# Kernel optimization log

Hardware: AMD Instinct MI355X
Metric: run time of the kernel (lower is better)

## Reference

```python
import jax, jax.numpy as jnp
import numpy as np

N_NODES = 100000
N_EDGES = 20000
N_PAIRS = 640000
IN_CH = 128
HEADS = 4
OUT_CH = 32


def setup_inputs() -> dict:
    key = jax.random.key(0)
    k1, k2, k3, k4, k5 = jax.random.split(key, 5)
    X = jax.random.normal(k1, (N_NODES, IN_CH), dtype=jnp.float32)
    # nn.Linear(in, H*C, bias=False); stored as [in, H*C] so X0 = X @ W
    W = jax.random.normal(k2, (IN_CH, HEADS * OUT_CH), dtype=jnp.float32) * (1.0 / np.sqrt(IN_CH))
    stdv = (6.0 / (HEADS + OUT_CH)) ** 0.5
    att_e = jax.random.uniform(k3, (1, HEADS, OUT_CH), dtype=jnp.float32, minval=-stdv, maxval=stdv)
    vertex = jax.random.randint(k4, (N_PAIRS,), 0, N_NODES, dtype=jnp.int64)
    edges = jax.random.randint(k5, (N_PAIRS,), 0, N_EDGES, dtype=jnp.int64)
    return {"X": X, "W": W, "att_e": att_e, "vertex": vertex, "edges": edges}


def reference(X, W, att_e, vertex, edges):
    N = X.shape[0]
    H, C = HEADS, OUT_CH
    X0 = X @ W                                  # [N, H*C]
    Xv_hc = X0.reshape(N, H, C)
    Xve = Xv_hc[vertex]                          # [M, H, C] gather
    # scatter-mean over hyperedges
    esum = jax.ops.segment_sum(Xve, edges, num_segments=N_EDGES)
    ecnt = jax.ops.segment_sum(jnp.ones((Xve.shape[0],), X.dtype), edges, num_segments=N_EDGES)
    Xe = esum / jnp.maximum(ecnt, 1.0)[:, None, None]   # [E, H, C]
    alpha_e = (Xe * att_e).sum(-1)               # [E, H]
    a_ev = alpha_e[edges]                        # [M, H]
    alpha = jax.nn.leaky_relu(a_ev, 0.01)
    # per-vertex softmax over incident hyperedges
    amax = jax.ops.segment_max(alpha, vertex, num_segments=N)
    alpha = jnp.exp(alpha - amax[vertex])
    asum = jax.ops.segment_sum(alpha, vertex, num_segments=N)
    alpha = alpha / (asum[vertex] + 1e-8)
    Xev = Xe[edges] * alpha[:, :, None]          # [M, H, C]
    Xv = jax.ops.segment_sum(Xev, vertex, num_segments=N)
    return Xv.reshape(N, H * C) + X0
```

## Files before the change

kernel.cpp:

```cpp
#include <hip/hip_runtime.h>
#include <hip/hip_bf16.h>

#define N_NODES 100000
#define N_EDGES 20000
#define N_PAIRS 640000
#define CH 128
#define HEADS 4
#define MAXDV 32

#define NG_GEMM 1563
#define NCHUNK 125
#define ECHUNK 5120
#define EW 5120
#define VWR 5000
#define NRANGE 5
#define VBIN_R 20000

#define OFF_X0H   0UL
#define OFF_XEH   25600000UL
#define OFF_LRE   30720000UL
#define OFF_LRV5  31360000UL
#define OFF_BLKE  34560000UL
#define OFF_BLKV  37120000UL
#define OFF_GSE   49620000UL
#define OFF_GSV   49722400UL
#define OFF_WT    50222400UL
#define OFF_ALPHA 50255168UL
#define OFF_OFFE  50575168UL
#define OFF_ENDE  50657088UL
#define OFF_OFFV  50739008UL
#define OFF_ENDV  51139008UL
#define OFF_PIDXE 51539008UL
#define OFF_PIDXV 54099008UL
#define OFF_TOT   56659008UL
#define ZERO_BYTES 8UL

typedef __attribute__((ext_vector_type(8))) short bf16x8;
typedef __attribute__((ext_vector_type(4))) float f32x4;

__device__ inline short f2bf(float f) {
    __hip_bfloat16 h = __float2bfloat16(f);
    return reinterpret_cast<short&>(h);
}
__device__ inline float bflo(unsigned w) { return __uint_as_float(w << 16); }
__device__ inline float bfhi(unsigned w) { return __uint_as_float(w & 0xffff0000u); }

__global__ __launch_bounds__(256) void k_wprep(const float* __restrict__ W,
                                               short* __restrict__ Wt) {
    const int idx = blockIdx.x * 256 + threadIdx.x;
    const int n = idx >> 7, k = idx & 127;
    Wt[n * CH + k] = f2bf(W[k * CH + n]);
}

__device__ inline void gemm_body(int gb, const float* __restrict__ X,
                                 const short* __restrict__ Wt,
                                 short* __restrict__ X0h) {
    const int t = threadIdx.x;
    const int wave = t >> 6, lane = t & 63;
    const int r0 = gb * 64 + (wave >> 1) * 32;
    const int c0 = (wave & 1) * 64;
    const int lrow = lane & 15, lk8 = (lane >> 4) * 8;
    const int row0 = min(r0 + lrow, N_NODES - 1);
    const int row1 = min(r0 + 16 + lrow, N_NODES - 1);
    const float* px0 = &X[(size_t)row0 * CH + lk8];
    const float* px1 = &X[(size_t)row1 * CH + lk8];
    const short* pw0 = &Wt[(size_t)(c0 + lrow) * CH + lk8];

    f32x4 acc[2][4] = {};

    float4 xa[2][2]; bf16x8 bb[4];
    xa[0][0] = *(const float4*)(px0); xa[0][1] = *(const float4*)(px0 + 4);
    xa[1][0] = *(const float4*)(px1); xa[1][1] = *(const float4*)(px1 + 4);
#pragma unroll
    for (int n = 0; n < 4; ++n) bb[n] = *(const bf16x8*)(pw0 + n * 16 * CH);

#pragma unroll
    for (int kk = 0; kk < 4; ++kk) {
        float4 xn[2][2]; bf16x8 bn[4];
        if (kk < 3) {
            const int ks = (kk + 1) * 32;
            xn[0][0] = *(const float4*)(px0 + ks); xn[0][1] = *(const float4*)(px0 + ks + 4);
            xn[1][0] = *(const float4*)(px1 + ks); xn[1][1] = *(const float4*)(px1 + ks + 4);
#pragma unroll
            for (int n = 0; n < 4; ++n) bn[n] = *(const bf16x8*)(pw0 + n * 16 * CH + ks);
        }
        bf16x8 a[2];
#pragma unroll
        for (int m = 0; m < 2; ++m) {
            a[m][0] = f2bf(xa[m][0].x); a[m][1] = f2bf(xa[m][0].y);
            a[m][2] = f2bf(xa[m][0].z); a[m][3] = f2bf(xa[m][0].w);
            a[m][4] = f2bf(xa[m][1].x); a[m][5] = f2bf(xa[m][1].y);
            a[m][6] = f2bf(xa[m][1].z); a[m][7] = f2bf(xa[m][1].w);
        }
#pragma unroll
        for (int m = 0; m < 2; ++m)
#pragma unroll
            for (int n = 0; n < 4; ++n)
                acc[m][n] = __builtin_amdgcn_mfma_f32_16x16x32_bf16(a[m], bb[n], acc[m][n], 0, 0, 0);
        if (kk < 3) {
#pragma unroll
            for (int m = 0; m < 2; ++m) { xa[m][0] = xn[m][0]; xa[m][1] = xn[m][1]; }
#pragma unroll
            for (int n = 0; n < 4; ++n) bb[n] = bn[n];
        }
    }

#pragma unroll
    for (int m = 0; m < 2; ++m) {
#pragma unroll
        for (int reg = 0; reg < 4; ++reg) {
            const int row = r0 + m * 16 + (lane >> 4) * 4 + reg;
            if (row < N_NODES) {
#pragma unroll
                for (int n = 0; n < 4; ++n)
                    X0h[(size_t)row * CH + c0 + n * 16 + (lane & 15)] = f2bf(acc[m][n][reg]);
            }
        }
    }
}

__global__ __launch_bounds__(256) void k_phase1(const float* __restrict__ X,
                                                const short* __restrict__ Wt,
                                                short* __restrict__ X0h,
                                                const int* __restrict__ vertex,
                                                const int* __restrict__ edges,
                                                unsigned char* __restrict__ lrank_e,
                                                unsigned char* __restrict__ lrank_v5,
                                                unsigned int* __restrict__ blkcnt_e,
                                                unsigned int* __restrict__ blkcnt_v) {
    __shared__ unsigned int hist[EW];
    const int bid = blockIdx.x;
    const int t = threadIdx.x;

    if (bid < NRANGE * NCHUNK) {
        const int r = bid % NRANGE, c = bid / NRANGE;
        for (int i = t; i < VWR; i += 256) hist[i] = 0;
        __syncthreads();
        const int base = c * ECHUNK;
        const int vmin = r * VBIN_R;
        unsigned char* __restrict__ lr = lrank_v5 + (size_t)r * N_PAIRS;
#pragma unroll
        for (int it = 0; it < 20; ++it) {
            const int m = base + it * 256 + t;
            const int loc = vertex[m] - vmin;
            if ((unsigned)loc < (unsigned)VBIN_R) {
                const unsigned sh = (unsigned)(loc & 3) * 8u;
                unsigned old = atomicAdd(&hist[loc >> 2], 1u << sh);
                lr[m] = (unsigned char)((old >> sh) & 0xffu);
            }
        }
        __syncthreads();
        unsigned int* dst = &blkcnt_v[(size_t)(r * NCHUNK + c) * VWR];
        for (int w = t; w < VWR; w += 256) dst[w] = hist[w];
        return;
    }
    if (bid < NRANGE * NCHUNK + NCHUNK) {
        const int c = bid - NRANGE * NCHUNK;
        for (int i = t; i < EW; i += 256) hist[i] = 0;
        __syncthreads();
        const int base = c * ECHUNK;
#pragma unroll
        for (int it = 0; it < 20; ++it) {
            const int m = base + it * 256 + t;
            const int e = edges[m];
            const unsigned sh = (unsigned)(e & 3) * 8u;
            unsigned old = atomicAdd(&hist[e >> 2], 1u << sh);
            lrank_e[m] = (unsigned char)((old >> sh) & 0xffu);
        }
        __syncthreads();
        unsigned int* dst = &blkcnt_e[(size_t)c * EW];
        for (int w = t; w < EW; w += 256) dst[w] = hist[w];
        return;
    }
    gemm_body(bid - (NRANGE * NCHUNK + NCHUNK), X, Wt, X0h);
}

__global__ __launch_bounds__(256) void k_scan_p1(const unsigned int* __restrict__ blkcnt_e,
                                                 const unsigned int* __restrict__ blkcnt_v,
                                                 unsigned int* __restrict__ gse,
                                                 unsigned int* __restrict__ gsv) {
    const int bid = blockIdx.x;
    if (bid < 25) {
        const int gid = bid * 256 + threadIdx.x;
        const int g = gid / 1280, w4 = gid % 1280;
        uint4 s = {0, 0, 0, 0};
#pragma unroll 5
        for (int i = 0; i < 25; ++i) {
            uint4 c = *(const uint4*)&blkcnt_e[(size_t)(g * 25 + i) * EW + w4 * 4];
            s.x += c.x; s.y += c.y; s.z += c.z; s.w += c.w;
        }
        *(uint4*)&gse[g * EW + w4 * 4] = s;
        return;
    }
    const int vid = (bid - 25) * 256 + threadIdx.x;
    if (vid >= 25 * (VWR / 4)) return;
    const int g = vid / (VWR / 4), w4 = vid % (VWR / 4);
    const int r = g / 5, cg = g % 5;
    uint4 s = {0, 0, 0, 0};
#pragma unroll 5
    for (int i = 0; i < 25; ++i) {
        uint4 c = *(const uint4*)&blkcnt_v[(size_t)(r * NCHUNK + cg * 25 + i) * VWR + w4 * 4];
        s.x += c.x; s.y += c.y; s.z += c.z; s.w += c.w;
    }
    *(uint4*)&gsv[g * VWR + w4 * 4] = s;
}

__global__ __launch_bounds__(256) void k_p2o(unsigned int* __restrict__ gse,
                                             unsigned int* __restrict__ gsv,
                                             int* __restrict__ off_e,
                                             int* __restrict__ end_e,
                                             int* __restrict__ off_v,
                                             int* __restrict__ end_v,
                                             int* __restrict__ totals) {
    __shared__ int s[256];
    __shared__ int base;
    const int bid = blockIdx.x, t = threadIdx.x;

    unsigned run = 0;
    int t0 = 0, t1 = 0, t2 = 0, t3 = 0;
    int binbase = -1;
    int* off; int* end; int* total;

    if (bid < 20) {
        const int w = bid * 256 + t;
#pragma unroll
        for (int g = 0; g < 5; ++g) {
            unsigned c = gse[g * EW + w];
            gse[g * EW + w] = run;
            run += c;
        }
        t0 = run & 255; t1 = (run >> 8) & 255; t2 = (run >> 16) & 255; t3 = run >> 24;
        binbase = 4 * w;
        off = off_e; end = end_e; total = &totals[0];
    } else {
        const int id = (bid - 20) * 256 + t;
        if (id < NRANGE * VWR) {
            const int r = id / VWR, w = id % VWR;
#pragma unroll
            for (int g = r * 5; g < r * 5 + 5; ++g) {
                unsigned c = gsv[g * VWR + w];
                gsv[g * VWR + w] = run;
                run += c;
            }
            t0 = run & 255; t1 = (run >> 8) & 255; t2 = (run >> 16) & 255; t3 = run >> 24;
            binbase = r * VBIN_R + 4 * w;
        }
        off = off_v; end = end_v; total = &totals[1];
    }

    const int mysum = t0 + t1 + t2 + t3;
    s[t] = mysum;
    __syncthreads();
    for (int d = 1; d < 256; d <<= 1) {
        int x = (t >= d) ? s[t - d] : 0;
        __syncthreads();
        s[t] += x;
        __syncthreads();
    }
    if (t == 0) base = atomicAdd(total, s[255]);
    __syncthreads();
    if (binbase >= 0) {
        int b = base + s[t] - mysum;
        off[binbase]     = b;           end[binbase]     = b + t0;  b += t0;
        off[binbase + 1] = b;           end[binbase + 1] = b + t1;  b += t1;
        off[binbase + 2] = b;           end[binbase + 2] = b + t2;  b += t2;
        off[binbase + 3] = b;           end[binbase + 3] = b + t3;
    }
}

__global__ __launch_bounds__(256) void k_scan_p3(unsigned int* __restrict__ blkcnt_e,
                                                 unsigned int* __restrict__ blkcnt_v,
                                                 const unsigned int* __restrict__ gse,
                                                 const unsigned int* __restrict__ gsv) {
    const int bid = blockIdx.x;
    if (bid < 25) {
        const int gid = bid * 256 + threadIdx.x;
        const int g = gid / 1280, w4 = gid % 1280;
        uint4 run = *(const uint4*)&gse[g * EW + w4 * 4];
#pragma unroll 5
        for (int i = 0; i < 25; ++i) {
            unsigned int* p = (unsigned int*)&blkcnt_e[(size_t)(g * 25 + i) * EW + w4 * 4];
            uint4 c = *(uint4*)p;
            *(uint4*)p = run;
            run.x += c.x; run.y += c.y; run.z += c.z; run.w += c.w;
        }
        return;
    }
    const int vid = (bid - 25) * 256 + threadIdx.x;
    if (vid >= 25 * (VWR / 4)) return;
    const int g = vid / (VWR / 4), w4 = vid % (VWR / 4);
    const int r = g / 5, cg = g % 5;
    uint4 run = *(const uint4*)&gsv[g * VWR + w4 * 4];
#pragma unroll 5
    for (int i = 0; i < 25; ++i) {
        unsigned int* p = (unsigned int*)&blkcnt_v[(size_t)(r * NCHUNK + cg * 25 + i) * VWR + w4 * 4];
        uint4 c = *(uint4*)p;
        *(uint4*)p = run;
        run.x += c.x; run.y += c.y; run.z += c.z; run.w += c.w;
    }
}

__global__ __launch_bounds__(256) void k_scatter(const int* __restrict__ vertex,
                                                 const int* __restrict__ edges,
                                                 const unsigned char* __restrict__ lrank_e,
                                                 const unsigned char* __restrict__ lrank_v5,
                                                 const unsigned int* __restrict__ blkcnt_e,
                                                 const unsigned int* __restrict__ blkcnt_v,
                                                 const int* __restrict__ off_e,
                                                 const int* __restrict__ off_v,
                                                 int* __restrict__ vlist_e,
                                                 int* __restrict__ elist_v) {
    const int m = blockIdx.x * 256 + threadIdx.x;
    const int e = edges[m];
    const int v = vertex[m];
    const int c = m / ECHUNK;
    const unsigned pe = blkcnt_e[(size_t)c * EW + (e >> 2)];
    const int er = (int)((pe >> ((unsigned)(e & 3) * 8u)) & 0xffu) + (int)lrank_e[m];
    const int r = v / VBIN_R, loc = v - r * VBIN_R;
    const unsigned pv = blkcnt_v[(size_t)(r * NCHUNK + c) * VWR + (loc >> 2)];
    const int vr = (int)((pv >> ((unsigned)(loc & 3) * 8u)) & 0xffu)
                 + (int)lrank_v5[(size_t)r * N_PAIRS + m];
    vlist_e[off_e[e] + er] = v;
    elist_v[off_v[v] + vr] = e;
}

__global__ __launch_bounds__(256) void k_edge(const short* __restrict__ X0h,
                                              const int* __restrict__ off_e,
                                              const int* __restrict__ end_e,
                                              const int* __restrict__ vlist,
                                              const float* __restrict__ att,
                                              short* __restrict__ Xeh,
                                              float* __restrict__ alpha_le) {
    const int t = threadIdx.x;
    const int slot = t >> 5, lane = t & 31;
    const int grp = lane >> 4, cl = lane & 15;
    const int e = blockIdx.x * 16 + slot * 2 + grp;
    const int s = off_e[e], en = end_e[e];
    const int deg = en - s;
    const short* __restrict__ xb = X0h + cl * 8;

    float va[8] = {0.f, 0.f, 0.f, 0.f, 0.f, 0.f, 0.f, 0.f};
    for (int c0 = 0; c0 < deg; c0 += 16) {
        const int cn = min(16, deg - c0);
        int vl = (cl < cn) ? (vlist[s + c0 + cl] << 7) : 0;
#pragma unroll 4
        for (int j = 0; j < cn; ++j) {
            const int vo = __shfl(vl, grp * 16 + j, 32);
            uint4 xq = *(const uint4*)(xb + vo);
            va[0] += bflo(xq.x); va[1] += bfhi(xq.x);
            va[2] += bflo(xq.y); va[3] += bfhi(xq.y);
            va[4] += bflo(xq.z); va[5] += bfhi(xq.z);
            va[6] += bflo(xq.w); va[7] += bfhi(xq.w);
        }
    }

    const float invd = 1.0f / fmaxf((float)deg, 1.0f);
    bf16x8 xh;
    float xe[8];
#pragma unroll
    for (int i = 0; i < 8; ++i) { xe[i] = va[i] * invd; xh[i] = f2bf(xe[i]); }
    *(bf16x8*)&Xeh[(size_t)e * CH + cl * 8] = xh;

    const float4 a0 = *(const float4*)&att[cl * 8];
    const float4 a1 = *(const float4*)&att[cl * 8 + 4];
    float p = xe[0] * a0.x + xe[1] * a0.y + xe[2] * a0.z + xe[3] * a0.w
            + xe[4] * a1.x + xe[5] * a1.y + xe[6] * a1.z + xe[7] * a1.w;
    p += __shfl_xor(p, 1);
    p += __shfl_xor(p, 2);
    if ((cl & 3) == 0) {
        alpha_le[e * HEADS + (cl >> 2)] = (p > 0.f) ? p : 0.01f * p;
    }
}

__global__ __launch_bounds__(256) void k_vertex(const short* __restrict__ X0h,
                                                const short* __restrict__ Xeh,
                                                const float* __restrict__ alpha_le,
                                                const int* __restrict__ off_v,
                                                const int* __restrict__ end_v,
                                                const int* __restrict__ elist,
                                                float* __restrict__ out) {
    const int t = threadIdx.x;
    const int slot = t >> 5, lane = t & 31;
    const int grp = lane >> 4, cl = lane & 15, h = cl >> 2;
    const int v = blockIdx.x * 16 + slot * 2 + grp;
    const int s = off_v[v], en = end_v[v];
    const int deg = en - s;

    __shared__ int   se[8][2][MAXDV];
    __shared__ float sa[8][2][MAXDV * HEADS];

    const short* __restrict__ xb = Xeh + cl * 8;

    float va[8] = {0.f, 0.f, 0.f, 0.f, 0.f, 0.f, 0.f, 0.f};
    if (deg <= MAXDV) {
        for (int j = cl; j < deg; j += 16) {
            const int e = elist[s + j];
            se[slot][grp][j] = e << 7;
            *(float4*)&sa[slot][grp][j << 2] = *(const float4*)&alpha_le[e * HEADS];
        }
        float mx = -INFINITY;
        for (int j = 0; j < deg; ++j) mx = fmaxf(mx, sa[slot][grp][(j << 2) + h]);
        float ssum = 0.f;
        for (int j = 0; j < deg; ++j) {
            const float p = __expf(sa[slot][grp][(j << 2) + h] - mx);
            sa[slot][grp][(j << 2) + h] = p;
            ssum += p;
        }
        const float inv = 1.0f / (ssum + 1e-8f);
        for (int j = 0; j < deg; ++j) {
            const float w = sa[slot][grp][(j << 2) + h] * inv;
            uint4 xq = *(const uint4*)(xb + se[slot][grp][j]);
            va[0] += w * bflo(xq.x); va[1] += w * bfhi(xq.x);
            va[2] += w * bflo(xq.y); va[3] += w * bfhi(xq.y);
            va[4] += w * bflo(xq.z); va[5] += w * bfhi(xq.z);
            va[6] += w * bflo(xq.w); va[7] += w * bfhi(xq.w);
        }
    } else {
        float mx = -INFINITY;
        for (int j = 0; j < deg; ++j) mx = fmaxf(mx, alpha_le[elist[s + j] * HEADS + h]);
        float ssum = 0.f;
        for (int j = 0; j < deg; ++j) ssum += __expf(alpha_le[elist[s + j] * HEADS + h] - mx);
        const float inv = 1.0f / (ssum + 1e-8f);
        for (int j = 0; j < deg; ++j) {
            const int e = elist[s + j];
            const float w = __expf(alpha_le[e * HEADS + h] - mx) * inv;
            uint4 xq = *(const uint4*)(xb + (e << 7));
            va[0] += w * bflo(xq.x); va[1] += w * bfhi(xq.x);
            va[2] += w * bflo(xq.y); va[3] += w * bfhi(xq.y);
            va[4] += w * bflo(xq.z); va[5] += w * bfhi(xq.z);
            va[6] += w * bflo(xq.w); va[7] += w * bfhi(xq.w);
        }
    }

    const uint4 rq = *(const uint4*)&X0h[(size_t)v * CH + cl * 8];
    float4 o0, o1;
    o0.x = va[0] + bflo(rq.x); o0.y = va[1] + bfhi(rq.x);
    o0.z = va[2] + bflo(rq.y); o0.w = va[3] + bfhi(rq.y);
    o1.x = va[4] + bflo(rq.z); o1.y = va[5] + bfhi(rq.z);
    o1.z = va[6] + bflo(rq.w); o1.w = va[7] + bfhi(rq.w);
    *(float4*)&out[(size_t)v * CH + cl * 8]     = o0;
    *(float4*)&out[(size_t)v * CH + cl * 8 + 4] = o1;
}

extern "C" void kernel_launch(void* const* d_in, const int* in_sizes, int n_in,
                              void* d_out, int out_size, void* d_ws, size_t ws_size,
                              hipStream_t stream) {
    const float* X      = (const float*)d_in[0];
    const float* W      = (const float*)d_in[1];
    const float* att    = (const float*)d_in[2];
    const int*   vertex = (const int*)d_in[3];
    const int*   edges  = (const int*)d_in[4];
    float* out = (float*)d_out;

    char* ws = (char*)d_ws;
    short* X0h      = (short*)(ws + OFF_X0H);
    short* Xeh      = (short*)(ws + OFF_XEH);
    unsigned char* lrank_e  = (unsigned char*)(ws + OFF_LRE);
    unsigned char* lrank_v5 = (unsigned char*)(ws + OFF_LRV5);
    unsigned int*  blkcnt_e = (unsigned int*)(ws + OFF_BLKE);
    unsigned int*  blkcnt_v = (unsigned int*)(ws + OFF_BLKV);
    unsigned int*  gse      = (unsigned int*)(ws + OFF_GSE);
    unsigned int*  gsv      = (unsigned int*)(ws + OFF_GSV);
    short* Wt       = (short*)(ws + OFF_WT);
    float* alpha_le = (float*)(ws + OFF_ALPHA);
    int* off_e   = (int*)(ws + OFF_OFFE);
    int* end_e   = (int*)(ws + OFF_ENDE);
    int* off_v   = (int*)(ws + OFF_OFFV);
    int* end_v   = (int*)(ws + OFF_ENDV);
    int* vlist_e = (int*)(ws + OFF_PIDXE);
    int* elist_v = (int*)(ws + OFF_PIDXV);
    int* totals  = (int*)(ws + OFF_TOT);

    hipMemsetAsync(ws + OFF_TOT, 0, ZERO_BYTES, stream);

    k_wprep<<<64, 256, 0, stream>>>(W, Wt);
    k_phase1<<<NRANGE * NCHUNK + NCHUNK + NG_GEMM, 256, 0, stream>>>(
        X, Wt, X0h, vertex, edges, lrank_e, lrank_v5, blkcnt_e, blkcnt_v);
    k_scan_p1<<<25 + 123, 256, 0, stream>>>(blkcnt_e, blkcnt_v, gse, gsv);
    k_p2o<<<20 + 98, 256, 0, stream>>>(gse, gsv, off_e, end_e, off_v, end_v, totals);
    k_scan_p3<<<25 + 123, 256, 0, stream>>>(blkcnt_e, blkcnt_v, gse, gsv);
    k_scatter<<<N_PAIRS / 256, 256, 0, stream>>>(vertex, edges, lrank_e, lrank_v5,
                                                 blkcnt_e, blkcnt_v, off_e, off_v,
                                                 vlist_e, elist_v);
    k_edge<<<N_EDGES / 16, 256, 0, stream>>>(X0h, off_e, end_e, vlist_e, att, Xeh, alpha_le);
    k_vertex<<<N_NODES / 16, 256, 0, stream>>>(X0h, Xeh, alpha_le, off_v, end_v, elist_v, out);
}
```

Baseline: 147.0 us.

## Merge three-pass chunk-count scan into one kernel and drop memset

Replaces the three-kernel hierarchical scan (partial group sums, group-level prefix, per-chunk write-back) with a single kernel where each thread serially scans all 125 chunk counts for its bin column. It also zeroes the totals counters inside k_wprep instead of issuing a separate memset. This removes two kernel launches and a memset plus the intermediate gse/gsv buffers. The cost is a longer serial dependent chain per thread across only 118 blocks, which lowers parallelism for the scan.

```diff
diff --git a/kernel.cpp b/kernel.cpp
--- a/kernel.cpp
+++ b/kernel.cpp
@@ -22,8 +22,6 @@
 #define OFF_LRV5  31360000UL
 #define OFF_BLKE  34560000UL
 #define OFF_BLKV  37120000UL
-#define OFF_GSE   49620000UL
-#define OFF_GSV   49722400UL
 #define OFF_WT    50222400UL
 #define OFF_ALPHA 50255168UL
 #define OFF_OFFE  50575168UL
@@ -33,7 +31,6 @@
 #define OFF_PIDXE 51539008UL
 #define OFF_PIDXV 54099008UL
 #define OFF_TOT   56659008UL
-#define ZERO_BYTES 8UL
 
 typedef __attribute__((ext_vector_type(8))) short bf16x8;
 typedef __attribute__((ext_vector_type(4))) float f32x4;
@@ -46,7 +43,9 @@
 __device__ inline float bfhi(unsigned w) { return __uint_as_float(w & 0xffff0000u); }
 
 __global__ __launch_bounds__(256) void k_wprep(const float* __restrict__ W,
-                                               short* __restrict__ Wt) {
+                                               short* __restrict__ Wt,
+                                               int* __restrict__ totals) {
+    if (blockIdx.x == 0 && threadIdx.x < 2) totals[threadIdx.x] = 0;
     const int idx = blockIdx.x * 256 + threadIdx.x;
     const int n = idx >> 7, k = idx & 127;
     Wt[n * CH + k] = f2bf(W[k * CH + n]);
@@ -175,79 +174,52 @@
     gemm_body(bid - (NRANGE * NCHUNK + NCHUNK), X, Wt, X0h);
 }
 
-__global__ __launch_bounds__(256) void k_scan_p1(const unsigned int* __restrict__ blkcnt_e,
-                                                 const unsigned int* __restrict__ blkcnt_v,
-                                                 unsigned int* __restrict__ gse,
-                                                 unsigned int* __restrict__ gsv) {
-    const int bid = blockIdx.x;
-    if (bid < 25) {
-        const int gid = bid * 256 + threadIdx.x;
-        const int g = gid / 1280, w4 = gid % 1280;
-        uint4 s = {0, 0, 0, 0};
-#pragma unroll 5
-        for (int i = 0; i < 25; ++i) {
-            uint4 c = *(const uint4*)&blkcnt_e[(size_t)(g * 25 + i) * EW + w4 * 4];
-            s.x += c.x; s.y += c.y; s.z += c.z; s.w += c.w;
-        }
-        *(uint4*)&gse[g * EW + w4 * 4] = s;
-        return;
-    }
-    const int vid = (bid - 25) * 256 + threadIdx.x;
-    if (vid >= 25 * (VWR / 4)) return;
-    const int g = vid / (VWR / 4), w4 = vid % (VWR / 4);
-    const int r = g / 5, cg = g % 5;
-    uint4 s = {0, 0, 0, 0};
-#pragma unroll 5
-    for (int i = 0; i < 25; ++i) {
-        uint4 c = *(const uint4*)&blkcnt_v[(size_t)(r * NCHUNK + cg * 25 + i) * VWR + w4 * 4];
-        s.x += c.x; s.y += c.y; s.z += c.z; s.w += c.w;
-    }
-    *(uint4*)&gsv[g * VWR + w4 * 4] = s;
-}
-
-__global__ __launch_bounds__(256) void k_p2o(unsigned int* __restrict__ gse,
-                                             unsigned int* __restrict__ gsv,
-                                             int* __restrict__ off_e,
-                                             int* __restrict__ end_e,
-                                             int* __restrict__ off_v,
-                                             int* __restrict__ end_v,
-                                             int* __restrict__ totals) {
+__global__ __launch_bounds__(256) void k_scan(unsigned int* __restrict__ blkcnt_e,
+                                              unsigned int* __restrict__ blkcnt_v,
+                                              int* __restrict__ off_e,
+                                              int* __restrict__ end_e,
+                                              int* __restrict__ off_v,
+                                              int* __restrict__ end_v,
+                                              int* __restrict__ totals) {
     __shared__ int s[256];
     __shared__ int base;
     const int bid = blockIdx.x, t = threadIdx.x;
 
     unsigned run = 0;
-    int t0 = 0, t1 = 0, t2 = 0, t3 = 0;
     int binbase = -1;
     int* off; int* end; int* total;
 
     if (bid < 20) {
         const int w = bid * 256 + t;
-#pragma unroll
-        for (int g = 0; g < 5; ++g) {
-            unsigned c = gse[g * EW + w];
-            gse[g * EW + w] = run;
-            run += c;
-        }
-        t0 = run & 255; t1 = (run >> 8) & 255; t2 = (run >> 16) & 255; t3 = run >> 24;
+        unsigned int* p = blkcnt_e + w;
+#pragma unroll 5
+        for (int c = 0; c < NCHUNK; ++c) {
+            const unsigned cc = *p;
+            *p = run;
+            run += cc;
+            p += EW;
+        }
         binbase = 4 * w;
         off = off_e; end = end_e; total = &totals[0];
     } else {
+        off = off_v; end = end_v; total = &totals[1];
         const int id = (bid - 20) * 256 + t;
         if (id < NRANGE * VWR) {
             const int r = id / VWR, w = id % VWR;
-#pragma unroll
-            for (int g = r * 5; g < r * 5 + 5; ++g) {
-                unsigned c = gsv[g * VWR + w];
-                gsv[g * VWR + w] = run;
-                run += c;
+            unsigned int* p = blkcnt_v + (size_t)r * NCHUNK * VWR + w;
+#pragma unroll 5
+            for (int c = 0; c < NCHUNK; ++c) {
+                const unsigned cc = *p;
+                *p = run;
+                run += cc;
+                p += VWR;
             }
-            t0 = run & 255; t1 = (run >> 8) & 255; t2 = (run >> 16) & 255; t3 = run >> 24;
             binbase = r * VBIN_R + 4 * w;
         }
-        off = off_v; end = end_v; total = &totals[1];
-    }
-
+    }
+
+    const int t0 = run & 255, t1 = (run >> 8) & 255,
+              t2 = (run >> 16) & 255, t3 = run >> 24;
     const int mysum = t0 + t1 + t2 + t3;
     s[t] = mysum;
     __syncthreads();
@@ -265,38 +237,6 @@
         off[binbase + 1] = b;           end[binbase + 1] = b + t1;  b += t1;
         off[binbase + 2] = b;           end[binbase + 2] = b + t2;  b += t2;
         off[binbase + 3] = b;           end[binbase + 3] = b + t3;
-    }
-}
-
-__global__ __launch_bounds__(256) void k_scan_p3(unsigned int* __restrict__ blkcnt_e,
-                                                 unsigned int* __restrict__ blkcnt_v,
-                                                 const unsigned int* __restrict__ gse,
-                                                 const unsigned int* __restrict__ gsv) {
-    const int bid = blockIdx.x;
-    if (bid < 25) {
-        const int gid = bid * 256 + threadIdx.x;
-        const int g = gid / 1280, w4 = gid % 1280;
-        uint4 run = *(const uint4*)&gse[g * EW + w4 * 4];
-#pragma unroll 5
-        for (int i = 0; i < 25; ++i) {
-            unsigned int* p = (unsigned int*)&blkcnt_e[(size_t)(g * 25 + i) * EW + w4 * 4];
-            uint4 c = *(uint4*)p;
-            *(uint4*)p = run;
-            run.x += c.x; run.y += c.y; run.z += c.z; run.w += c.w;
-        }
-        return;
-    }
-    const int vid = (bid - 25) * 256 + threadIdx.x;
-    if (vid >= 25 * (VWR / 4)) return;
-    const int g = vid / (VWR / 4), w4 = vid % (VWR / 4);
-    const int r = g / 5, cg = g % 5;
-    uint4 run = *(const uint4*)&gsv[g * VWR + w4 * 4];
-#pragma unroll 5
-    for (int i = 0; i < 25; ++i) {
-        unsigned int* p = (unsigned int*)&blkcnt_v[(size_t)(r * NCHUNK + cg * 25 + i) * VWR + w4 * 4];
-        uint4 c = *(uint4*)p;
-        *(uint4*)p = run;
-        run.x += c.x; run.y += c.y; run.z += c.z; run.w += c.w;
     }
 }
 
@@ -459,8 +399,6 @@
     unsigned char* lrank_v5 = (unsigned char*)(ws + OFF_LRV5);
     unsigned int*  blkcnt_e = (unsigned int*)(ws + OFF_BLKE);
     unsigned int*  blkcnt_v = (unsigned int*)(ws + OFF_BLKV);
-    unsigned int*  gse      = (unsigned int*)(ws + OFF_GSE);
-    unsigned int*  gsv      = (unsigned int*)(ws + OFF_GSV);
     short* Wt       = (short*)(ws + OFF_WT);
     float* alpha_le = (float*)(ws + OFF_ALPHA);
     int* off_e   = (int*)(ws + OFF_OFFE);
@@ -471,14 +409,11 @@
     int* elist_v = (int*)(ws + OFF_PIDXV);
     int* totals  = (int*)(ws + OFF_TOT);
 
-    hipMemsetAsync(ws + OFF_TOT, 0, ZERO_BYTES, stream);
-
-    k_wprep<<<64, 256, 0, stream>>>(W, Wt);
+    k_wprep<<<64, 256, 0, stream>>>(W, Wt, totals);
     k_phase1<<<NRANGE * NCHUNK + NCHUNK + NG_GEMM, 256, 0, stream>>>(
         X, Wt, X0h, vertex, edges, lrank_e, lrank_v5, blkcnt_e, blkcnt_v);
-    k_scan_p1<<<25 + 123, 256, 0, stream>>>(blkcnt_e, blkcnt_v, gse, gsv);
-    k_p2o<<<20 + 98, 256, 0, stream>>>(gse, gsv, off_e, end_e, off_v, end_v, totals);
-    k_scan_p3<<<25 + 123, 256, 0, stream>>>(blkcnt_e, blkcnt_v, gse, gsv);
+    k_scan<<<20 + 98, 256, 0, stream>>>(blkcnt_e, blkcnt_v, off_e, end_e,
+                                        off_v, end_v, totals);
     k_scatter<<<N_PAIRS / 256, 256, 0, stream>>>(vertex, edges, lrank_e, lrank_v5,
                                                  blkcnt_e, blkcnt_v, off_e, off_v,
                                                  vlist_e, elist_v);
```

Measured after the change: 144.5 us. No clear change (-1.8%).
